# Performance work log

Hardware: AMD Instinct MI355X
Metric: run time of the kernel (lower is better)

## Reference

```python
import jax, jax.numpy as jnp
import numpy as np

K = 8  # search_range in sample_wise_recolor
BIG = 1e30


def setup_inputs() -> dict:
    key = jax.random.key(0)
    ks = jax.random.split(key, 6)
    L, N = 16384, 10000  # L: upsampled candidate voxels (multiple of 8), N: target points
    pred_F = jax.random.normal(ks[0], (L,), jnp.float32)
    cand_xyz = jax.random.normal(ks[1], (L, 3), jnp.float32) * 50.0
    cand_rgb = jax.random.uniform(ks[2], (L, 3), jnp.float32)
    tgt_xyz = jax.random.normal(ks[3], (N, 3), jnp.float32) * 50.0
    tgt_rgb = jax.random.uniform(ks[4], (N, 3), jnp.float32)
    keep_target = jax.random.randint(ks[5], (L,), 0, 2, jnp.int32)
    return {"pred_F": pred_F, "cand_xyz": cand_xyz, "cand_rgb": cand_rgb,
            "tgt_xyz": tgt_xyz, "tgt_rgb": tgt_rgb, "keep_target": keep_target,
            "points_num": 8192}


def _get_keep(pred, points_num):
    # local-max mask over groups of 8 children (scatter of per-row argmax)
    L = pred.shape[0]
    p8 = pred.reshape(-1, 8)
    rows = jnp.arange(p8.shape[0])
    is_local_max = jnp.zeros(p8.shape, dtype=bool).at[rows, jnp.argmax(p8, axis=1)].set(True).reshape(-1)
    # kthvalue over the non-local-max subset: local-max entries pushed to +inf so the
    # k-th smallest of the full sorted array equals the k-th smallest of the subset.
    k = L - points_num  # static python int
    vals = jnp.where(is_local_max, jnp.inf, pred)
    threshold = jnp.sort(vals)[k - 1]
    return (pred > threshold) | is_local_max


def _pairwise_sqdist(a, b):
    # a: [P,3], b: [Q,3] -> [P,Q] squared distances
    a2 = jnp.sum(a * a, axis=1)
    b2 = jnp.sum(b * b, axis=1)
    d2 = a2[:, None] + b2[None, :] - 2.0 * (a @ b.T)
    return jnp.maximum(d2, 0.0)


def _recolor_loss(cand_xyz, rgb, keep, tgt_xyz, tgt_rgb):
    L = cand_xyz.shape[0]
    N = tgt_xyz.shape[0]
    d2 = _pairwise_sqdist(tgt_xyz, cand_xyz)  # [N, L]

    # ---- recolor_backward: KNN from each target point into kept candidates ----
    d_masked = jnp.where(keep[None, :], d2, BIG)
    neg_d, idx = jax.lax.top_k(-d_masked, K)  # [N, K]
    d = -neg_d
    zero_mask = d == 0.0
    min_mask = (d == jnp.min(d, axis=1, keepdims=True)) & ~jnp.any(zero_mask, axis=1)[:, None]
    w = jnp.where(min_mask, 1.0 / jnp.sqrt(jnp.maximum(d, 1e-30)), 0.0)  # [N, K]

    flat_idx = idx.reshape(-1)
    num = jnp.zeros((L, 3), rgb.dtype).at[flat_idx].add((tgt_rgb[:, None, :] * w[:, :, None]).reshape(-1, 3))
    den = jnp.zeros((L,), rgb.dtype).at[flat_idx].add(w.reshape(-1))
    has_den = den != 0.0
    recolored = jnp.where(has_den[:, None], num / jnp.where(has_den, den, 1.0)[:, None], 0.0)

    # exact-match (zero-distance) targets overwrite; scatter with safe out-of-range dummy row
    safe_idx = jnp.where(zero_mask, idx, L).reshape(-1)
    tgt_exp = jnp.broadcast_to(tgt_rgb[:, None, :], (N, K, 3)).reshape(-1, 3)
    recolored = jnp.concatenate([recolored, jnp.zeros((1, 3), rgb.dtype)], 0).at[safe_idx].set(tgt_exp)[:L]
    empty = jnp.concatenate([~has_den, jnp.zeros((1,), bool)], 0).at[safe_idx].set(False)[:L]
    empty = empty & keep  # only kept candidates matter

    # ---- recolor_forward: kept candidates with no color yet pull from nearest targets ----
    neg_df, idxf = jax.lax.top_k(-d2.T, K)  # [L, K]
    df = -neg_df
    mf = df == jnp.min(df, axis=1, keepdims=True)
    rec_fwd = jnp.sum(tgt_rgb[idxf] * mf[:, :, None], axis=1) / jnp.sum(mf, axis=1, keepdims=True).astype(rgb.dtype)
    recolored = jnp.where(empty[:, None], rec_fwd, recolored)

    # L1 loss over kept candidates only; recolor target is no-grad in the original
    recolored = jax.lax.stop_gradient(recolored)
    return jnp.sum(jnp.where(keep[:, None], jnp.abs(rgb - recolored), 0.0))


def reference(pred_F, cand_xyz, cand_rgb, tgt_xyz, tgt_rgb, keep_target, points_num):
    keep = _get_keep(jax.lax.stop_gradient(pred_F), points_num)  # @torch.no_grad
    # coord recon loss: BCE-with-logits, reduction='sum'
    t = keep_target.astype(pred_F.dtype)
    coord_loss = jnp.sum(jnp.maximum(pred_F, 0.0) - pred_F * t + jnp.log1p(jnp.exp(-jnp.abs(pred_F))))
    # inverse_transform_for_color in training mode: x * 255
    rgb = cand_rgb * 255.0
    rgb_loss = _recolor_loss(cand_xyz, rgb, keep, tgt_xyz, tgt_rgb)
    return jnp.stack([coord_loss, rgb_loss])
```

## Files before the change

kernel.cpp:

```cpp
#include <hip/hip_runtime.h>
#include <hip/hip_bf16.h>


#define CH 1024
typedef unsigned long long ull;

__global__ __launch_bounds__(256) void k_prep(
    const float* __restrict__ pred, const float* __restrict__ txyz,
    float4* __restrict__ ttile, float4* __restrict__ numden,
    int* __restrict__ zerohit, unsigned int* __restrict__ key,
    unsigned char* __restrict__ islm, int* __restrict__ counters,
    float* __restrict__ out, int L, int N) {
  int gidx = blockIdx.x * 256 + threadIdx.x;
  int gsz = (int)gridDim.x * 256;
  for (int i = gidx; i < N; i += gsz) {
    float x = txyz[3*i], y = txyz[3*i+1], z = txyz[3*i+2];
    ttile[i] = make_float4(x, y, z, fmaf(x, x, fmaf(y, y, z * z)));
  }
  for (int i = gidx; i < L; i += gsz) {
    numden[i] = make_float4(0.f, 0.f, 0.f, 0.f);
    zerohit[i] = 0;
  }
  if (gidx < 8) counters[gidx] = 0;
  if (gidx < 2) out[gidx] = 0.f;
  int ngroups = L >> 3;
  for (int g = gidx; g < ngroups; g += gsz) {
    const float4* pv = (const float4*)pred + (size_t)g * 2;
    float4 a = pv[0], b = pv[1];
    float v[8] = {a.x, a.y, a.z, a.w, b.x, b.y, b.z, b.w};
    int bi = 0; float bv = v[0];
    #pragma unroll
    for (int j = 1; j < 8; ++j) if (v[j] > bv) { bv = v[j]; bi = j; }
    unsigned int kk[8];
    ull lmpack = 0ull;
    #pragma unroll
    for (int j = 0; j < 8; ++j) {
      unsigned int fb = __float_as_uint(v[j]);
      unsigned int mk = (fb & 0x80000000u) ? ~fb : (fb | 0x80000000u);
      if (j == bi) { mk = 0xFF800000u; lmpack |= 1ull << (8 * j); }
      kk[j] = mk;
    }
    ((uint4*)key)[g*2]   = make_uint4(kk[0], kk[1], kk[2], kk[3]);
    ((uint4*)key)[g*2+1] = make_uint4(kk[4], kk[5], kk[6], kk[7]);
    *(ull*)(islm + (size_t)g * 8) = lmpack;
  }
}

__device__ __forceinline__ void select_bin(
    unsigned int* hist, int nb, unsigned int rank,
    unsigned int* sB, unsigned int* sR, int tid) {
  if (tid < 64) {
    int g = nb >> 6;
    unsigned int sum = 0;
    for (int j = 0; j < g; ++j) sum += hist[tid * g + j];
    unsigned int incl = sum;
    for (int o = 1; o < 64; o <<= 1) {
      unsigned int v = __shfl_up(incl, o);
      if (tid >= o) incl += v;
    }
    unsigned int excl = incl - sum;
    bool cond = (rank >= excl) && (rank < incl);
    unsigned long long bal = __ballot(cond);
    int first = __ffsll((long long)bal) - 1;
    if (tid == first) {
      unsigned int r = rank - excl, cum = 0;
      for (int j = 0; j < g; ++j) {
        unsigned int c = hist[tid * g + j];
        if (r < cum + c) { *sB = (unsigned int)(tid * g + j); *sR = r - cum; break; }
        cum += c;
      }
    }
  }
}

__global__ __launch_bounds__(256) void k_sel(
    const unsigned int* __restrict__ key, const int* __restrict__ pnum_p,
    float* __restrict__ thr_out, int L) {
  __shared__ unsigned int hist[2048];
  __shared__ unsigned int sB, sR;
  int tid = threadIdx.x;
  unsigned int rank = (unsigned int)(L - pnum_p[0] - 1);
  const uint4* k4 = (const uint4*)key;
  int n4 = L >> 2;
  for (int b = tid; b < 2048; b += 256) hist[b] = 0u;
  __syncthreads();
  for (int i = tid; i < n4; i += 256) {
    uint4 v = k4[i];
    atomicAdd(&hist[v.x >> 21], 1u); atomicAdd(&hist[v.y >> 21], 1u);
    atomicAdd(&hist[v.z >> 21], 1u); atomicAdd(&hist[v.w >> 21], 1u);
  }
  __syncthreads();
  select_bin(hist, 2048, rank, &sB, &sR, tid);
  __syncthreads();
  unsigned int B1 = sB, R1 = sR;
  for (int b = tid; b < 2048; b += 256) hist[b] = 0u;
  __syncthreads();
  for (int i = tid; i < n4; i += 256) {
    uint4 v = k4[i];
    if ((v.x >> 21) == B1) atomicAdd(&hist[(v.x >> 10) & 2047u], 1u);
    if ((v.y >> 21) == B1) atomicAdd(&hist[(v.y >> 10) & 2047u], 1u);
    if ((v.z >> 21) == B1) atomicAdd(&hist[(v.z >> 10) & 2047u], 1u);
    if ((v.w >> 21) == B1) atomicAdd(&hist[(v.w >> 10) & 2047u], 1u);
  }
  __syncthreads();
  select_bin(hist, 2048, R1, &sB, &sR, tid);
  __syncthreads();
  unsigned int B2 = sB, R2 = sR;
  for (int b = tid; b < 1024; b += 256) hist[b] = 0u;
  __syncthreads();
  unsigned int top22 = (B1 << 11) | B2;
  for (int i = tid; i < n4; i += 256) {
    uint4 v = k4[i];
    if ((v.x >> 10) == top22) atomicAdd(&hist[v.x & 1023u], 1u);
    if ((v.y >> 10) == top22) atomicAdd(&hist[v.y & 1023u], 1u);
    if ((v.z >> 10) == top22) atomicAdd(&hist[v.z & 1023u], 1u);
    if ((v.w >> 10) == top22) atomicAdd(&hist[v.w & 1023u], 1u);
  }
  __syncthreads();
  select_bin(hist, 1024, R2, &sB, &sR, tid);
  __syncthreads();
  if (tid == 0) {
    unsigned int fkey = (B1 << 21) | (B2 << 10) | sB;
    unsigned int fb = (fkey & 0x80000000u) ? (fkey & 0x7FFFFFFFu) : ~fkey;
    thr_out[0] = __uint_as_float(fb);
  }
}

__global__ __launch_bounds__(256) void k_keepc(
    const float* __restrict__ pred, const unsigned char* __restrict__ islm,
    const float* __restrict__ thr_p, const float* __restrict__ cxyz,
    const int* __restrict__ ktgt, int* __restrict__ keep,
    float4* __restrict__ klist, int* __restrict__ kidx,
    int* __restrict__ counters, float* __restrict__ out, int L) {
  int i = blockIdx.x * 256 + threadIdx.x;
  float thr = thr_p[0];
  float term = 0.f;
  if (i < L) {
    float p = pred[i];
    bool kp = (p > thr) || islm[i];
    keep[i] = kp ? 1 : 0;
    if (kp) {
      int pos = atomicAdd(&counters[0], 1);
      float x = cxyz[3*i], y = cxyz[3*i+1], z = cxyz[3*i+2];
      klist[pos] = make_float4(x, y, z, fmaf(x, x, fmaf(y, y, z * z)));
      kidx[pos] = i;
    }
    float t = (float)ktgt[i];
    term = fmaxf(p, 0.f) - p * t + log1pf(expf(-fabsf(p)));
  }
  for (int o = 32; o > 0; o >>= 1) term += __shfl_down(term, o);
  if ((threadIdx.x & 63) == 0) atomicAdd(&out[0], term);
}

__global__ __launch_bounds__(256) void k_scanw(
    const float* __restrict__ txyz, const float4* __restrict__ klist,
    const int* __restrict__ kidx, const float4* __restrict__ ttile,
    const int* __restrict__ counters, ull* __restrict__ tmin,
    int* __restrict__ fidx, int L, int N, int NBW) {
  __shared__ float4 sb[CH];
  int tid = threadIdx.x;
  int lane = tid & 63;
  int wv = tid >> 6;
  int kc = counters[0];
  int bid = blockIdx.x;

  float q0x, q0y, q0z, q1x, q1y, q1z, q2x, q2y, q2z, q3x, q3y, q3z;
  const float4* list; int listn; int q0;
  if (bid < NBW) {
    q0 = bid * 16 + wv * 4;
    int a = min(q0, N - 1), b = min(q0 + 1, N - 1),
        c = min(q0 + 2, N - 1), d = min(q0 + 3, N - 1);
    q0x = txyz[3*a]; q0y = txyz[3*a+1]; q0z = txyz[3*a+2];
    q1x = txyz[3*b]; q1y = txyz[3*b+1]; q1z = txyz[3*b+2];
    q2x = txyz[3*c]; q2y = txyz[3*c+1]; q2z = txyz[3*c+2];
    q3x = txyz[3*d]; q3y = txyz[3*d+1]; q3z = txyz[3*d+2];
    list = klist; listn = kc;
  } else {
    int eb = (bid - NBW) * 16;
    if (eb >= kc) return;
    q0 = eb + wv * 4;
    int a = min(q0, kc - 1), b = min(q0 + 1, kc - 1),
        c = min(q0 + 2, kc - 1), d = min(q0 + 3, kc - 1);
    float4 A = klist[a], B = klist[b], C = klist[c], D = klist[d];
    q0x = A.x; q0y = A.y; q0z = A.z;
    q1x = B.x; q1y = B.y; q1z = B.z;
    q2x = C.x; q2y = C.y; q2z = C.z;
    q3x = D.x; q3y = D.y; q3z = D.z;
    list = ttile; listn = N;
  }
  float n0x = -2.f*q0x, n0y = -2.f*q0y, n0z = -2.f*q0z;
  float n1x = -2.f*q1x, n1y = -2.f*q1y, n1z = -2.f*q1z;
  float n2x = -2.f*q2x, n2y = -2.f*q2y, n2z = -2.f*q2z;
  float n3x = -2.f*q3x, n3y = -2.f*q3y, n3z = -2.f*q3z;
  float b0 = 3e38f, b1 = 3e38f, b2 = 3e38f, b3 = 3e38f;
  int i0 = 0, i1 = 0, i2 = 0, i3 = 0;

  for (int tile = 0; tile < listn; tile += CH) {
    int cnt = min(CH, listn - tile);
    int cntp = (cnt + 63) & ~63;
    for (int j = tid; j < cntp; j += 256)
      sb[j] = (j < cnt) ? list[tile + j] : make_float4(0.f, 0.f, 0.f, 3e38f);
    __syncthreads();
    #pragma unroll 2
    for (int i = lane; i < cntp; i += 64) {
      float4 A = sb[i];
      int c = tile + i;
      float d0 = fmaf(n0x, A.x, A.w); d0 = fmaf(n0y, A.y, d0); d0 = fmaf(n0z, A.z, d0);
      float d1 = fmaf(n1x, A.x, A.w); d1 = fmaf(n1y, A.y, d1); d1 = fmaf(n1z, A.z, d1);
      float d2 = fmaf(n2x, A.x, A.w); d2 = fmaf(n2y, A.y, d2); d2 = fmaf(n2z, A.z, d2);
      float d3 = fmaf(n3x, A.x, A.w); d3 = fmaf(n3y, A.y, d3); d3 = fmaf(n3z, A.z, d3);
      if (d0 < b0) { b0 = d0; i0 = c; }
      if (d1 < b1) { b1 = d1; i1 = c; }
      if (d2 < b2) { b2 = d2; i2 = c; }
      if (d3 < b3) { b3 = d3; i3 = c; }
    }
    __syncthreads();
  }
  #pragma unroll
  for (int o = 32; o > 0; o >>= 1) {
    float ob; int oi;
    ob = __shfl_xor(b0, o); oi = __shfl_xor(i0, o);
    if (ob < b0 || (ob == b0 && oi < i0)) { b0 = ob; i0 = oi; }
    ob = __shfl_xor(b1, o); oi = __shfl_xor(i1, o);
    if (ob < b1 || (ob == b1 && oi < i1)) { b1 = ob; i1 = oi; }
    ob = __shfl_xor(b2, o); oi = __shfl_xor(i2, o);
    if (ob < b2 || (ob == b2 && oi < i2)) { b2 = ob; i2 = oi; }
    ob = __shfl_xor(b3, o); oi = __shfl_xor(i3, o);
    if (ob < b3 || (ob == b3 && oi < i3)) { b3 = ob; i3 = oi; }
  }
  if (lane == 0) {
    int ii[4] = {i0, i1, i2, i3};
    if (bid < NBW) {
      #pragma unroll
      for (int j = 0; j < 4; ++j) {
        int t = q0 + j;
        if (t < N) {
          float4 cd = klist[ii[j]];
          float dx = txyz[3*t] - cd.x, dy = txyz[3*t+1] - cd.y, dz = txyz[3*t+2] - cd.z;
          float dtrue = fmaf(dx, dx, fmaf(dy, dy, dz * dz));
          tmin[t] = ((ull)__float_as_uint(dtrue) << 32) | (unsigned int)kidx[ii[j]];
        }
      }
    } else {
      #pragma unroll
      for (int j = 0; j < 4; ++j) {
        int e = q0 + j;
        if (e < kc) fidx[kidx[e]] = ii[j];
      }
    }
  }
}

__global__ __launch_bounds__(256) void k_scatter(
    const float* __restrict__ trgb, const ull* __restrict__ tmin,
    float4* __restrict__ numden, int* __restrict__ zerohit,
    float4* __restrict__ zcolor, int N) {
  int t = blockIdx.x * 256 + threadIdx.x;
  if (t >= N) return;
  ull pack = tmin[t];
  float d = __uint_as_float((unsigned int)(pack >> 32));
  int idx = (int)(pack & 0xFFFFFFFFull);
  float r = trgb[3*t], g = trgb[3*t+1], b = trgb[3*t+2];
  if (d == 0.0f) {
    zerohit[idx] = 1;
    zcolor[idx] = make_float4(r, g, b, 0.f);
  } else {
    float w = 1.0f / sqrtf(fmaxf(d, 1e-30f));
    atomicAdd(&numden[idx].x, r * w);
    atomicAdd(&numden[idx].y, g * w);
    atomicAdd(&numden[idx].z, b * w);
    atomicAdd(&numden[idx].w, w);
  }
}

__global__ __launch_bounds__(256) void k_loss(
    const float* __restrict__ crgb, const float* __restrict__ trgb,
    const int* __restrict__ keep, const float4* __restrict__ numden,
    const int* __restrict__ zerohit, const float4* __restrict__ zcolor,
    const int* __restrict__ fidx, float* __restrict__ out, int L) {
  int l = blockIdx.x * 256 + threadIdx.x;
  float loss = 0.f;
  if (l < L && keep[l]) {
    float rr, rg, rb;
    if (zerohit[l]) {
      float4 z = zcolor[l]; rr = z.x; rg = z.y; rb = z.z;
    } else {
      float4 nd = numden[l];
      if (nd.w != 0.f) { rr = nd.x / nd.w; rg = nd.y / nd.w; rb = nd.z / nd.w; }
      else {
        int ti = fidx[l];
        rr = trgb[3*ti]; rg = trgb[3*ti+1]; rb = trgb[3*ti+2];
      }
    }
    float sr = crgb[3*l]*255.f, sg = crgb[3*l+1]*255.f, sb = crgb[3*l+2]*255.f;
    loss = fabsf(sr - rr) + fabsf(sg - rg) + fabsf(sb - rb);
  }
  for (int o = 32; o > 0; o >>= 1) loss += __shfl_down(loss, o);
  if ((threadIdx.x & 63) == 0) atomicAdd(&out[1], loss);
}

extern "C" void kernel_launch(void* const* d_in, const int* in_sizes, int n_in,
                              void* d_out, int out_size, void* d_ws, size_t ws_size,
                              hipStream_t stream) {
  const float* pred = (const float*)d_in[0];
  const float* cxyz = (const float*)d_in[1];
  const float* crgb = (const float*)d_in[2];
  const float* txyz = (const float*)d_in[3];
  const float* trgb = (const float*)d_in[4];
  const int*   ktgt = (const int*)d_in[5];
  const int*   pnum = (const int*)d_in[6];
  int L = in_sizes[0];
  int N = in_sizes[3] / 3;

  char* ws = (char*)d_ws;
  size_t off = 0;
  float4* klist  = (float4*)(ws + off);   off += (size_t)L * 16;
  float4* ttile  = (float4*)(ws + off);   off += (size_t)((N + 3) & ~3) * 16;
  float4* numden = (float4*)(ws + off);   off += (size_t)L * 16;
  float4* zcolor = (float4*)(ws + off);   off += (size_t)L * 16;
  unsigned int* key = (unsigned int*)(ws + off); off += (size_t)L * 4;
  ull* tmin      = (ull*)(ws + off);      off += (size_t)((N + 1) & ~1) * 8;
  int* keep      = (int*)(ws + off);      off += (size_t)L * 4;
  int* kidx      = (int*)(ws + off);      off += (size_t)L * 4;
  int* zerohit   = (int*)(ws + off);      off += (size_t)L * 4;
  int* fidx      = (int*)(ws + off);      off += (size_t)L * 4;
  float* thr_slot = (float*)(ws + off);   off += 16;
  int* counters  = (int*)(ws + off);      off += 256;
  unsigned char* islm = (unsigned char*)(ws + off); off += ((size_t)L + 15) & ~15ull;
  float* out = (float*)d_out;

  int nbL = (L + 255) / 256;
  int nbN = (N + 255) / 256;
  int NBW = (N + 15) / 16;
  int NFW = (L + 15) / 16;
  int mx = max(L, N);

  k_prep<<<(mx + 255) / 256, 256, 0, stream>>>(
      pred, txyz, ttile, numden, zerohit, key, islm, counters, out, L, N);

  k_sel<<<1, 256, 0, stream>>>(key, pnum, thr_slot, L);

  k_keepc<<<nbL, 256, 0, stream>>>(
      pred, islm, thr_slot, cxyz, ktgt, keep, klist, kidx, counters, out, L);

  k_scanw<<<NBW + NFW, 256, 0, stream>>>(
      txyz, klist, kidx, ttile, counters, tmin, fidx, L, N, NBW);

  k_scatter<<<nbN, 256, 0, stream>>>(trgb, tmin, numden, zerohit, zcolor, N);

  k_loss<<<nbL, 256, 0, stream>>>(
      crgb, trgb, keep, numden, zerohit, zcolor, fidx, out, L);
}
```

Baseline: 144.1 us.

## Drop LDS staging in NN scan and process 8 queries per wave

The nearest-neighbour scan kernel no longer stages candidate tiles in shared memory with block barriers. Each wave now streams the list straight from global memory (through cache), two entries per iteration. Each wave handles 8 queries instead of 4, which doubles arithmetic reuse per loaded point and halves the block count. This removes the __syncthreads overhead and LDS traffic, but it relies on L1/L2 serving the repeated global reads and raises register pressure.

```diff
diff --git a/kernel.cpp b/kernel.cpp
--- a/kernel.cpp
+++ b/kernel.cpp
@@ -2,7 +2,6 @@
 #include <hip/hip_bf16.h>
 
 
-#define CH 1024
 typedef unsigned long long ull;
 
 __global__ __launch_bounds__(256) void k_prep(
@@ -157,82 +156,81 @@
     const int* __restrict__ kidx, const float4* __restrict__ ttile,
     const int* __restrict__ counters, ull* __restrict__ tmin,
     int* __restrict__ fidx, int L, int N, int NBW) {
-  __shared__ float4 sb[CH];
   int tid = threadIdx.x;
   int lane = tid & 63;
   int wv = tid >> 6;
   int kc = counters[0];
   int bid = blockIdx.x;
 
-  float q0x, q0y, q0z, q1x, q1y, q1z, q2x, q2y, q2z, q3x, q3y, q3z;
   const float4* list; int listn; int q0;
+  float qx[8], qy[8], qz[8];
   if (bid < NBW) {
-    q0 = bid * 16 + wv * 4;
-    int a = min(q0, N - 1), b = min(q0 + 1, N - 1),
-        c = min(q0 + 2, N - 1), d = min(q0 + 3, N - 1);
-    q0x = txyz[3*a]; q0y = txyz[3*a+1]; q0z = txyz[3*a+2];
-    q1x = txyz[3*b]; q1y = txyz[3*b+1]; q1z = txyz[3*b+2];
-    q2x = txyz[3*c]; q2y = txyz[3*c+1]; q2z = txyz[3*c+2];
-    q3x = txyz[3*d]; q3y = txyz[3*d+1]; q3z = txyz[3*d+2];
+    q0 = (bid * 4 + wv) * 8;
+    #pragma unroll
+    for (int j = 0; j < 8; ++j) {
+      int a = min(q0 + j, N - 1);
+      qx[j] = txyz[3*a]; qy[j] = txyz[3*a+1]; qz[j] = txyz[3*a+2];
+    }
     list = klist; listn = kc;
   } else {
-    int eb = (bid - NBW) * 16;
+    int eb = (bid - NBW) * 32;
     if (eb >= kc) return;
-    q0 = eb + wv * 4;
-    int a = min(q0, kc - 1), b = min(q0 + 1, kc - 1),
-        c = min(q0 + 2, kc - 1), d = min(q0 + 3, kc - 1);
-    float4 A = klist[a], B = klist[b], C = klist[c], D = klist[d];
-    q0x = A.x; q0y = A.y; q0z = A.z;
-    q1x = B.x; q1y = B.y; q1z = B.z;
-    q2x = C.x; q2y = C.y; q2z = C.z;
-    q3x = D.x; q3y = D.y; q3z = D.z;
+    q0 = eb + wv * 8;
+    #pragma unroll
+    for (int j = 0; j < 8; ++j) {
+      int a = min(q0 + j, kc - 1);
+      float4 A = klist[a];
+      qx[j] = A.x; qy[j] = A.y; qz[j] = A.z;
+    }
     list = ttile; listn = N;
   }
-  float n0x = -2.f*q0x, n0y = -2.f*q0y, n0z = -2.f*q0z;
-  float n1x = -2.f*q1x, n1y = -2.f*q1y, n1z = -2.f*q1z;
-  float n2x = -2.f*q2x, n2y = -2.f*q2y, n2z = -2.f*q2z;
-  float n3x = -2.f*q3x, n3y = -2.f*q3y, n3z = -2.f*q3z;
-  float b0 = 3e38f, b1 = 3e38f, b2 = 3e38f, b3 = 3e38f;
-  int i0 = 0, i1 = 0, i2 = 0, i3 = 0;
-
-  for (int tile = 0; tile < listn; tile += CH) {
-    int cnt = min(CH, listn - tile);
-    int cntp = (cnt + 63) & ~63;
-    for (int j = tid; j < cntp; j += 256)
-      sb[j] = (j < cnt) ? list[tile + j] : make_float4(0.f, 0.f, 0.f, 3e38f);
-    __syncthreads();
-    #pragma unroll 2
-    for (int i = lane; i < cntp; i += 64) {
-      float4 A = sb[i];
-      int c = tile + i;
-      float d0 = fmaf(n0x, A.x, A.w); d0 = fmaf(n0y, A.y, d0); d0 = fmaf(n0z, A.z, d0);
-      float d1 = fmaf(n1x, A.x, A.w); d1 = fmaf(n1y, A.y, d1); d1 = fmaf(n1z, A.z, d1);
-      float d2 = fmaf(n2x, A.x, A.w); d2 = fmaf(n2y, A.y, d2); d2 = fmaf(n2z, A.z, d2);
-      float d3 = fmaf(n3x, A.x, A.w); d3 = fmaf(n3y, A.y, d3); d3 = fmaf(n3z, A.z, d3);
-      if (d0 < b0) { b0 = d0; i0 = c; }
-      if (d1 < b1) { b1 = d1; i1 = c; }
-      if (d2 < b2) { b2 = d2; i2 = c; }
-      if (d3 < b3) { b3 = d3; i3 = c; }
-    }
-    __syncthreads();
-  }
+  float nx[8], ny[8], nz[8], bb[8]; int ii[8];
+  #pragma unroll
+  for (int j = 0; j < 8; ++j) {
+    nx[j] = -2.f * qx[j]; ny[j] = -2.f * qy[j]; nz[j] = -2.f * qz[j];
+    bb[j] = 3e38f; ii[j] = 0;
+  }
+
+  int i = lane;
+  for (; i + 64 < listn; i += 128) {
+    float4 A = list[i];
+    float4 B = list[i + 64];
+    #pragma unroll
+    for (int j = 0; j < 8; ++j) {
+      float dA = fmaf(nx[j], A.x, A.w);
+      dA = fmaf(ny[j], A.y, dA);
+      dA = fmaf(nz[j], A.z, dA);
+      if (dA < bb[j]) { bb[j] = dA; ii[j] = i; }
+      float dB = fmaf(nx[j], B.x, B.w);
+      dB = fmaf(ny[j], B.y, dB);
+      dB = fmaf(nz[j], B.z, dB);
+      if (dB < bb[j]) { bb[j] = dB; ii[j] = i + 64; }
+    }
+  }
+  if (i < listn) {
+    float4 A = list[i];
+    #pragma unroll
+    for (int j = 0; j < 8; ++j) {
+      float dA = fmaf(nx[j], A.x, A.w);
+      dA = fmaf(ny[j], A.y, dA);
+      dA = fmaf(nz[j], A.z, dA);
+      if (dA < bb[j]) { bb[j] = dA; ii[j] = i; }
+    }
+  }
+
   #pragma unroll
   for (int o = 32; o > 0; o >>= 1) {
-    float ob; int oi;
-    ob = __shfl_xor(b0, o); oi = __shfl_xor(i0, o);
-    if (ob < b0 || (ob == b0 && oi < i0)) { b0 = ob; i0 = oi; }
-    ob = __shfl_xor(b1, o); oi = __shfl_xor(i1, o);
-    if (ob < b1 || (ob == b1 && oi < i1)) { b1 = ob; i1 = oi; }
-    ob = __shfl_xor(b2, o); oi = __shfl_xor(i2, o);
-    if (ob < b2 || (ob == b2 && oi < i2)) { b2 = ob; i2 = oi; }
-    ob = __shfl_xor(b3, o); oi = __shfl_xor(i3, o);
-    if (ob < b3 || (ob == b3 && oi < i3)) { b3 = ob; i3 = oi; }
+    #pragma unroll
+    for (int j = 0; j < 8; ++j) {
+      float ob = __shfl_xor(bb[j], o);
+      int   oi = __shfl_xor(ii[j], o);
+      if (ob < bb[j] || (ob == bb[j] && oi < ii[j])) { bb[j] = ob; ii[j] = oi; }
+    }
   }
   if (lane == 0) {
-    int ii[4] = {i0, i1, i2, i3};
     if (bid < NBW) {
       #pragma unroll
-      for (int j = 0; j < 4; ++j) {
+      for (int j = 0; j < 8; ++j) {
         int t = q0 + j;
         if (t < N) {
           float4 cd = klist[ii[j]];
@@ -243,7 +241,7 @@
       }
     } else {
       #pragma unroll
-      for (int j = 0; j < 4; ++j) {
+      for (int j = 0; j < 8; ++j) {
         int e = q0 + j;
         if (e < kc) fidx[kidx[e]] = ii[j];
       }
@@ -331,8 +329,8 @@
 
   int nbL = (L + 255) / 256;
   int nbN = (N + 255) / 256;
-  int NBW = (N + 15) / 16;
-  int NFW = (L + 15) / 16;
+  int NBW = (N + 31) / 32;
+  int NFW = (L + 31) / 32;
   int mx = max(L, N);
 
   k_prep<<<(mx + 255) / 256, 256, 0, stream>>>(
```

After: 147.7 us. 2.5% more time.
